# Performance work log

Measured on AMD Instinct MI355X. Metric: run time of the kernel, lower is better.

## Reference

```python
import jax, jax.numpy as jnp
import numpy as np

KERNEL_SIZE = 3
STRIDE = 1
DILATE = 1
EPS = 1e-12  # torch F.normalize default eps


def _center_indices(height, width):
    half = KERNEL_SIZE // 2
    ys, xs = [], []
    for y_idx in range(half + DILATE - 1, height - half - DILATE + 1, STRIDE):
        for x_idx in range(half + DILATE - 1, width - half - DILATE + 1, STRIDE):
            ys.append(y_idx)
            xs.append(x_idx)
    return np.asarray(ys), np.asarray(xs)


def _offsets():
    half = KERNEL_SIZE // 2
    offs = []
    for dy in range(-(half + DILATE) + 1, half + DILATE, DILATE):
        for dx in range(-(half + DILATE) + 1, half + DILATE, DILATE):
            offs.append((dy, dx))
    return offs


def setup_inputs() -> dict:
    key = jax.random.key(0)
    k0, k1, k2, k3, k4 = jax.random.split(key, 5)
    B, C, H, W, HS = 8, 512, 14, 14, 1024
    x = jax.random.normal(k0, (B, C, H, W), dtype=jnp.float32)
    w1 = jax.random.normal(k1, (HS, C), dtype=jnp.float32) * 0.02
    b1 = jax.random.normal(k2, (HS,), dtype=jnp.float32) * 0.02
    w2 = jax.random.normal(k3, (HS, C), dtype=jnp.float32) * 0.02
    b2 = jax.random.normal(k4, (HS,), dtype=jnp.float32) * 0.02
    return {"x": x, "w1": w1, "b1": b1, "w2": w2, "b2": b2}


def reference(x, w1, b1, w2, b2):
    B, C, H, W = x.shape
    ys, xs = _center_indices(H, W)  # static numpy indices, K = len(ys)
    offs = _offsets()               # 9 neighbor offsets

    # center pixels -> fc1: [B, K, HS]
    center = x[:, :, ys, xs]                                  # [B, C, K]
    center_proj = jnp.einsum('bck,hc->bkh', center, w1) + b1  # [B, K, HS]

    # gather all 9 neighbor sets at once: [O, B, C, K]
    sides = jnp.stack([x[:, :, ys + dy, xs + dx] for dy, dx in offs], axis=0)
    side_proj = jnp.einsum('obck,hc->obkh', sides, w2) + b2   # [O, B, K, HS]

    # outer-product sum-pooled over K: [B, O, HS, HS]
    cofe = jnp.einsum('bki,obkj->boij', center_proj, side_proj)

    # L2 normalize over last dim (torch F.normalize semantics)
    norm = jnp.sqrt(jnp.sum(cofe * cofe, axis=-1, keepdims=True))
    return cofe / jnp.maximum(norm, EPS)
```

## Files before the change

### kernel.cpp

```cpp
#include <hip/hip_runtime.h>
#include <hip/hip_bf16.h>
#include <cstdint>
#include <cstddef>

typedef __attribute__((ext_vector_type(8))) short short8;
typedef __attribute__((ext_vector_type(16))) float float16;


static __device__ __forceinline__ unsigned short f2bf(float f) {
  union { float f; unsigned int u; } v; v.f = f;
  unsigned int r = v.u + 0x7fffu + ((v.u >> 16) & 1u);
  return (unsigned short)(r >> 16);
}

__global__ __launch_bounds__(256, 2)
void proj_kernel(const float* __restrict__ x,
                 const float* __restrict__ w1, const float* __restrict__ b1,
                 const float* __restrict__ w2, const float* __restrict__ b2,
                 unsigned short* __restrict__ P)
{
  const int nt = blockIdx.x;
  const int mt = blockIdx.y;
  const int b  = blockIdx.z;
  const int mat = (mt >= 8) ? 1 : 0;
  const float* __restrict__ w    = mat ? w2 : w1;
  const float* __restrict__ bias = mat ? b2 : b1;
  const int h0 = (mt - mat * 8) * 128;
  const int p0 = nt * 64;

  __shared__ unsigned short As[128 * 72];
  __shared__ unsigned short Bs[64 * 72];

  const int tid  = threadIdx.x;
  const int lane = tid & 63, wave = tid >> 6;
  const int ln31 = lane & 31, lh = lane >> 5;

  float16 acc0, acc1;
  #pragma unroll
  for (int r = 0; r < 16; ++r) { acc0[r] = 0.f; acc1[r] = 0.f; }

  for (int kc = 0; kc < 512; kc += 64) {
    #pragma unroll
    for (int i = 0; i < 8; ++i) {
      int idx = tid + i * 256;
      int row = idx >> 4;
      int c4  = (idx & 15) << 2;
      const float4 v = *(const float4*)&w[(size_t)(h0 + row) * 512 + kc + c4];
      unsigned short* dst = &As[row * 72 + c4];
      dst[0] = f2bf(v.x); dst[1] = f2bf(v.y); dst[2] = f2bf(v.z); dst[3] = f2bf(v.w);
    }
    #pragma unroll
    for (int i = 0; i < 16; ++i) {
      int idx = tid + i * 256;
      int c  = idx >> 6;
      int pl = idx & 63;
      int p  = p0 + pl;
      float val = 0.f;
      if (p < 196) val = x[((size_t)b * 512 + kc + c) * 196 + p];
      Bs[pl * 72 + c] = f2bf(val);
    }
    __syncthreads();
    #pragma unroll
    for (int ks = 0; ks < 4; ++ks) {
      short8 a   = *(const short8*)&As[(wave * 32 + ln31) * 72 + ks * 16 + lh * 8];
      short8 bb0 = *(const short8*)&Bs[(ln31) * 72 + ks * 16 + lh * 8];
      short8 bb1 = *(const short8*)&Bs[(32 + ln31) * 72 + ks * 16 + lh * 8];
      acc0 = __builtin_amdgcn_mfma_f32_32x32x16_bf16(a, bb0, acc0, 0, 0, 0);
      acc1 = __builtin_amdgcn_mfma_f32_32x32x16_bf16(a, bb1, acc1, 0, 0, 0);
    }
    __syncthreads();
  }

  #pragma unroll
  for (int r = 0; r < 16; ++r) {
    int rowl = (r & 3) + ((r >> 2) << 3) + (lh << 2);
    int h = h0 + wave * 32 + rowl;
    float bi = bias[h];
    size_t base = ((size_t)(mat * 8 + b) * 1024 + h) * 196;
    int p_a = p0 + ln31;
    if (p_a < 196) P[base + p_a] = f2bf(acc0[r] + bi);
    int p_b = p_a + 32;
    if (p_b < 196) P[base + p_b] = f2bf(acc1[r] + bi);
  }
}

__global__ __launch_bounds__(256)
void gather_kernel(const unsigned short* __restrict__ P,
                   unsigned short* __restrict__ cpz,
                   unsigned short* __restrict__ spz)
{
  const int idx = blockIdx.x * 256 + threadIdx.x;
  const unsigned short* P2 = P + (size_t)8 * 1024 * 196;
  unsigned short tmp[8];
  if (idx < 147456) {
    int h  = idx & 1;
    int t  = idx >> 1;
    int i  = t & 1023;
    int t2 = t >> 10;
    int s  = t2 % 9;
    int b  = t2 / 9;
    int kbase = s * 16 + h * 8;
    const unsigned short* src = P + ((size_t)b * 1024 + i) * 196;
    #pragma unroll
    for (int e = 0; e < 8; ++e) {
      int k = kbase + e;
      int ky = k / 12, kx = k % 12;
      tmp[e] = src[(ky + 1) * 14 + (kx + 1)];
    }
    *(uint4*)(cpz + (size_t)idx * 8) = *(const uint4*)tmp;
  } else {
    int j2 = idx - 147456;
    int h  = j2 & 1;
    int t  = j2 >> 1;
    int j  = t & 1023;
    int t2 = t >> 10;
    int s  = t2 % 9;
    int t3 = t2 / 9;
    int b  = t3 & 7;
    int o  = t3 >> 3;
    int dy = o / 3 - 1, dx = o % 3 - 1;
    int kbase = s * 16 + h * 8;
    const unsigned short* src = P2 + ((size_t)b * 1024 + j) * 196;
    #pragma unroll
    for (int e = 0; e < 8; ++e) {
      int k = kbase + e;
      int ky = k / 12, kx = k % 12;
      tmp[e] = src[(ky + 1 + dy) * 14 + (kx + 1 + dx)];
    }
    *(uint4*)(spz + (size_t)j2 * 8) = *(const uint4*)tmp;
  }
}

__global__ __launch_bounds__(256, 2)
void cofe_kernel(const unsigned short* __restrict__ cpz,
                 const unsigned short* __restrict__ spz,
                 float* __restrict__ out)
{
  const int iblk = blockIdx.x;
  const int o    = blockIdx.y;
  const int b    = blockIdx.z;
  const int tid  = threadIdx.x;
  const int lane = tid & 63, wave = tid >> 6;
  const int ln31 = lane & 31, lh = lane >> 5;
  const int i0 = iblk << 5;
  const int jw = wave << 8;

  float16 acc[8];
  #pragma unroll
  for (int t = 0; t < 8; ++t) {
    #pragma unroll
    for (int r = 0; r < 16; ++r) acc[t][r] = 0.f;
  }

  const uint4* A  = (const uint4*)cpz;
  const uint4* Bp = (const uint4*)spz;
  const size_t abase = ((size_t)b * 9 * 1024 + i0 + ln31) * 2 + lh;
  const size_t bbase = ((size_t)(o * 8 + b) * 9 * 1024 + jw + ln31) * 2 + lh;

  #pragma unroll
  for (int s = 0; s < 9; ++s) {
    short8 a = *(const short8*)(A + abase + (size_t)s * 2048);
    #pragma unroll
    for (int t = 0; t < 8; ++t) {
      short8 bb = *(const short8*)(Bp + bbase + (size_t)s * 2048 + t * 64);
      acc[t] = __builtin_amdgcn_mfma_f32_32x32x16_bf16(a, bb, acc[t], 0, 0, 0);
    }
  }

  float ssq[16];
  #pragma unroll
  for (int r = 0; r < 16; ++r) {
    float s2 = 0.f;
    #pragma unroll
    for (int t = 0; t < 8; ++t) s2 += acc[t][r] * acc[t][r];
    ssq[r] = s2;
  }
  #pragma unroll
  for (int m = 1; m <= 16; m <<= 1) {
    #pragma unroll
    for (int r = 0; r < 16; ++r) ssq[r] += __shfl_xor(ssq[r], m, 64);
  }

  __shared__ float s_ssq[32];
  if (tid < 32) s_ssq[tid] = 0.f;
  __syncthreads();
  if (ln31 == 0) {
    #pragma unroll
    for (int r = 0; r < 16; ++r) {
      int rowl = (r & 3) + ((r >> 2) << 3) + (lh << 2);
      atomicAdd(&s_ssq[rowl], ssq[r]);
    }
  }
  __syncthreads();

  const size_t outbase = ((size_t)(b * 9 + o) << 20) + ((size_t)i0 << 10) + jw + ln31;
  #pragma unroll
  for (int r = 0; r < 16; ++r) {
    int rowl = (r & 3) + ((r >> 2) << 3) + (lh << 2);
    float nrm = sqrtf(s_ssq[rowl]);
    float sc = 1.f / fmaxf(nrm, 1e-12f);
    size_t rb = outbase + ((size_t)rowl << 10);
    #pragma unroll
    for (int t = 0; t < 8; ++t)
      out[rb + (t << 5)] = acc[t][r] * sc;
  }
}

extern "C" void kernel_launch(void* const* d_in, const int* in_sizes, int n_in,
                              void* d_out, int out_size, void* d_ws, size_t ws_size,
                              hipStream_t stream)
{
  const float* x  = (const float*)d_in[0];
  const float* w1 = (const float*)d_in[1];
  const float* b1 = (const float*)d_in[2];
  const float* w2 = (const float*)d_in[3];
  const float* b2 = (const float*)d_in[4];
  float* out = (float*)d_out;

  unsigned short* P   = (unsigned short*)d_ws;
  unsigned short* cpz = P + (size_t)2 * 8 * 1024 * 196;
  unsigned short* spz = cpz + (size_t)8 * 9 * 1024 * 16;

  proj_kernel<<<dim3(4, 16, 8), 256, 0, stream>>>(x, w1, b1, w2, b2, P);
  gather_kernel<<<dim3(5760), 256, 0, stream>>>(P, cpz, spz);
  cofe_kernel<<<dim3(32, 9, 8), 256, 0, stream>>>(cpz, spz, out);
}
```

Before: 414.8 us.

## Stage gather rows in LDS, widen cofe blocks, use nontemporal output stores

Measured after the change: 431.7 us. 1.04x slower.

```diff
diff --git a/kernel.cpp b/kernel.cpp
--- a/kernel.cpp
+++ b/kernel.cpp
@@ -89,49 +89,65 @@
                    unsigned short* __restrict__ cpz,
                    unsigned short* __restrict__ spz)
 {
-  const int idx = blockIdx.x * 256 + threadIdx.x;
-  const unsigned short* P2 = P + (size_t)8 * 1024 * 196;
+  const int jt   = blockIdx.x;
+  const int task = blockIdx.y;
+  const int b    = blockIdx.z;
+  const int tid  = threadIdx.x;
+  const int j0   = jt * 32;
+
+  __shared__ unsigned short rows[32 * 200];
+  __shared__ unsigned short pos0[144];
+  __shared__ unsigned short pad_[8];
+
+  if (tid < 144) {
+    int ky = tid / 12, kx = tid % 12;
+    pos0[tid] = (unsigned short)((ky + 1) * 14 + (kx + 1));
+  }
+  (void)pad_;
+
+  const unsigned short* src =
+      P + ((size_t)(task * 8 + b) * 1024 + j0) * 196;
+  const unsigned int* src32 = (const unsigned int*)src;
+  #pragma unroll
+  for (int i = 0; i < 13; ++i) {
+    int idx = tid + i * 256;
+    if (idx < 3136) {
+      int row = idx / 98;
+      int c   = idx - row * 98;
+      ((unsigned int*)&rows[row * 200])[c] = src32[idx];
+    }
+  }
+  __syncthreads();
+
   unsigned short tmp[8];
-  if (idx < 147456) {
-    int h  = idx & 1;
-    int t  = idx >> 1;
-    int i  = t & 1023;
-    int t2 = t >> 10;
-    int s  = t2 % 9;
-    int b  = t2 / 9;
-    int kbase = s * 16 + h * 8;
-    const unsigned short* src = P + ((size_t)b * 1024 + i) * 196;
-    #pragma unroll
-    for (int e = 0; e < 8; ++e) {
-      int k = kbase + e;
-      int ky = k / 12, kx = k % 12;
-      tmp[e] = src[(ky + 1) * 14 + (kx + 1)];
-    }
-    *(uint4*)(cpz + (size_t)idx * 8) = *(const uint4*)tmp;
+  if (task == 0) {
+    for (int t = tid; t < 576; t += 256) {
+      int h = t & 1, row = (t >> 1) & 31, s = t >> 6;
+      int kb = s * 16 + h * 8;
+      const unsigned short* rp = &rows[row * 200];
+      short8 ps = *(const short8*)&pos0[kb];
+      #pragma unroll
+      for (int e = 0; e < 8; ++e) tmp[e] = rp[(unsigned short)ps[e]];
+      size_t chunk = ((size_t)(b * 9 + s) * 1024 + j0 + row) * 2 + h;
+      *(uint4*)(cpz + chunk * 8) = *(const uint4*)tmp;
+    }
   } else {
-    int j2 = idx - 147456;
-    int h  = j2 & 1;
-    int t  = j2 >> 1;
-    int j  = t & 1023;
-    int t2 = t >> 10;
-    int s  = t2 % 9;
-    int t3 = t2 / 9;
-    int b  = t3 & 7;
-    int o  = t3 >> 3;
-    int dy = o / 3 - 1, dx = o % 3 - 1;
-    int kbase = s * 16 + h * 8;
-    const unsigned short* src = P2 + ((size_t)b * 1024 + j) * 196;
-    #pragma unroll
-    for (int e = 0; e < 8; ++e) {
-      int k = kbase + e;
-      int ky = k / 12, kx = k % 12;
-      tmp[e] = src[(ky + 1 + dy) * 14 + (kx + 1 + dx)];
-    }
-    *(uint4*)(spz + (size_t)j2 * 8) = *(const uint4*)tmp;
-  }
-}
-
-__global__ __launch_bounds__(256, 2)
+    for (int t = tid; t < 5184; t += 256) {
+      int h = t & 1, row = (t >> 1) & 31, q = t >> 6;
+      int o = q / 9, s = q - o * 9;
+      int doff = (o / 3 - 1) * 14 + (o % 3 - 1);
+      int kb = s * 16 + h * 8;
+      const unsigned short* rp = &rows[row * 200];
+      short8 ps = *(const short8*)&pos0[kb];
+      #pragma unroll
+      for (int e = 0; e < 8; ++e) tmp[e] = rp[(unsigned short)ps[e] + doff];
+      size_t chunk = (((size_t)(o * 8 + b) * 9 + s) * 1024 + j0 + row) * 2 + h;
+      *(uint4*)(spz + chunk * 8) = *(const uint4*)tmp;
+    }
+  }
+}
+
+__global__ __launch_bounds__(512, 2)
 void cofe_kernel(const unsigned short* __restrict__ cpz,
                  const unsigned short* __restrict__ spz,
                  float* __restrict__ out)
@@ -142,8 +158,8 @@
   const int tid  = threadIdx.x;
   const int lane = tid & 63, wave = tid >> 6;
   const int ln31 = lane & 31, lh = lane >> 5;
-  const int i0 = iblk << 5;
-  const int jw = wave << 8;
+  const int istrip = (iblk << 6) + ((wave >> 2) << 5);
+  const int jw = (wave & 3) << 8;
 
   float16 acc[8];
   #pragma unroll
@@ -154,7 +170,7 @@
 
   const uint4* A  = (const uint4*)cpz;
   const uint4* Bp = (const uint4*)spz;
-  const size_t abase = ((size_t)b * 9 * 1024 + i0 + ln31) * 2 + lh;
+  const size_t abase = ((size_t)b * 9 * 1024 + istrip + ln31) * 2 + lh;
   const size_t bbase = ((size_t)(o * 8 + b) * 9 * 1024 + jw + ln31) * 2 + lh;
 
   #pragma unroll
@@ -181,28 +197,30 @@
     for (int r = 0; r < 16; ++r) ssq[r] += __shfl_xor(ssq[r], m, 64);
   }
 
-  __shared__ float s_ssq[32];
-  if (tid < 32) s_ssq[tid] = 0.f;
+  __shared__ float s_ssq[64];
+  if (tid < 64) s_ssq[tid] = 0.f;
   __syncthreads();
   if (ln31 == 0) {
+    int rbase = (wave >> 2) << 5;
     #pragma unroll
     for (int r = 0; r < 16; ++r) {
       int rowl = (r & 3) + ((r >> 2) << 3) + (lh << 2);
-      atomicAdd(&s_ssq[rowl], ssq[r]);
+      atomicAdd(&s_ssq[rbase + rowl], ssq[r]);
     }
   }
   __syncthreads();
 
-  const size_t outbase = ((size_t)(b * 9 + o) << 20) + ((size_t)i0 << 10) + jw + ln31;
+  const size_t outbase = ((size_t)(b * 9 + o) << 20) + ((size_t)istrip << 10) + jw + ln31;
+  const int rbase = (wave >> 2) << 5;
   #pragma unroll
   for (int r = 0; r < 16; ++r) {
     int rowl = (r & 3) + ((r >> 2) << 3) + (lh << 2);
-    float nrm = sqrtf(s_ssq[rowl]);
+    float nrm = sqrtf(s_ssq[rbase + rowl]);
     float sc = 1.f / fmaxf(nrm, 1e-12f);
     size_t rb = outbase + ((size_t)rowl << 10);
     #pragma unroll
     for (int t = 0; t < 8; ++t)
-      out[rb + (t << 5)] = acc[t][r] * sc;
+      __builtin_nontemporal_store(acc[t][r] * sc, &out[rb + (t << 5)]);
   }
 }
 
@@ -222,6 +240,6 @@
   unsigned short* spz = cpz + (size_t)8 * 9 * 1024 * 16;
 
   proj_kernel<<<dim3(4, 16, 8), 256, 0, stream>>>(x, w1, b1, w2, b2, P);
-  gather_kernel<<<dim3(5760), 256, 0, stream>>>(P, cpz, spz);
-  cofe_kernel<<<dim3(32, 9, 8), 256, 0, stream>>>(cpz, spz, out);
-}
+  gather_kernel<<<dim3(32, 2, 8), 256, 0, stream>>>(P, cpz, spz);
+  cofe_kernel<<<dim3(16, 9, 8), 512, 0, stream>>>(cpz, spz, out);
+}
```
